# Kernel tuning notes

Measured on AMD Instinct MI355X. Metric: run time of the kernel, lower is better.

The kernel has to match this reference:

```python
import jax, jax.numpy as jnp
from jax import lax
import numpy as np

B, V, H, K, E = 256, 30000, 512, 200, 300
SH_ALPHA = 20.0
REC_W = 0.7
N_ITERS = 100       # fixed iteration budget (original caps at 5000; convergence check freezes updates)
STOP_THR = 0.005
BN_EPS = 1e-3


def setup_inputs() -> dict:
    key = jax.random.key(0)
    ks = jax.random.split(key, 8)
    n = lambda k, shape, scale: (jax.random.normal(k, shape, jnp.float32) * scale)
    return {
        "bows": jax.random.uniform(ks[0], (B, V), jnp.float32),
        "W1": n(ks[1], (H, V), 0.01),
        "b1": jnp.zeros((H,), jnp.float32),
        "W2": n(ks[2], (K, H), 0.05),
        "b2": jnp.zeros((K,), jnp.float32),
        "gamma": jnp.ones((K,), jnp.float32),
        "beta": jnp.zeros((K,), jnp.float32),
        "word_emb": n(ks[3], (V, E), 0.1),
        "topic_emb": n(ks[4], (K, E), 0.1),
    }


def _l2norm(x):
    return x / jnp.maximum(jnp.linalg.norm(x, axis=1, keepdims=True), 1e-12)


def _sinkhorn(cost, kernel, a, b):
    # a: [K,B], b: [V,B], kernel: [K,V]
    u0 = jnp.ones_like(a) / a.shape[0]
    v0 = jnp.ones_like(b)

    def body(carry, i):
        u, v, err = carry
        active = err > STOP_THR
        # u = a / (kernel @ (b / (u^T kernel)^T))
        u1 = a / (kernel @ (b / (u.T @ kernel).T))

        def check(_):
            v1 = b / (kernel.T @ u1)
            u2 = a / (kernel @ v1)
            bb = v1 * (kernel.T @ u2)
            e = jnp.max(jnp.sum(jnp.abs(bb - b), axis=0))
            return u2, v1, e

        # original does the v-refresh + err check when steps % 20 == 1 (steps = i+1)
        u1, v1, e1 = lax.cond(i % 20 == 0, check, lambda _: (u1, v, err), None)
        u = jnp.where(active, u1, u)
        v = jnp.where(active, v1, v)
        err = jnp.where(active, e1, err)
        return (u, v, err), None

    (u, v, _), _ = lax.scan(jax.checkpoint(body), (u0, v0, jnp.asarray(1.0, a.dtype)),
                            jnp.arange(N_ITERS))
    # per-document sinkhorn cost: sum_k u * ((kernel*cost) @ v)
    return jnp.sum(u * ((kernel * cost) @ v), axis=0)  # [B]


def reference(bows, W1, b1, W2, b2, gamma, beta, word_emb, topic_emb):
    # encoder (training-mode BN with batch stats; dropout disabled for determinism)
    h = jax.nn.relu(bows @ W1.T + b1)                      # [B,H]
    z = h @ W2.T + b2                                      # [B,K]
    mu = jnp.mean(z, axis=0)
    var = jnp.var(z, axis=0)                               # biased, as torch BN uses
    zn = gamma * (z - mu) / jnp.sqrt(var + BN_EPS) + beta
    doc_topic = jax.nn.softmax(zn, axis=1)                 # [B,K]

    topic_word = _l2norm(topic_emb) @ _l2norm(word_emb).T  # [K,V]
    cost = 1.0 - topic_word
    kernel = jnp.exp(-cost * SH_ALPHA)

    doc_word = jax.nn.softmax(bows, axis=1)                # [B,V]
    sinkhorn_loss = _sinkhorn(cost, kernel, doc_topic.T, doc_word.T).mean()

    rec_log_probs = jax.nn.log_softmax(doc_topic @ topic_word, axis=1)  # [B,V]
    reconstruction_loss = -(rec_log_probs * bows).sum(axis=1).mean()
    return REC_W * reconstruction_loss, sinkhorn_loss
```

## Files before the change

kernel.cpp:

```cpp
#include <hip/hip_runtime.h>
#include <math.h>

#define CDIV(a,b) (((a)+(b)-1)/(b))

typedef unsigned short u16;
typedef unsigned long long u64;
typedef __attribute__((ext_vector_type(8))) short bf16x8;
typedef __attribute__((ext_vector_type(4))) float f32x4;

constexpr int Bn = 256;
constexpr int Vn = 30000;
constexpr int Hn = 512;
constexpr int Kn = 200;
constexpr int En = 300;
constexpr int E3 = 320;
constexpr int Kp = 224;
constexpr int Vc = 224;
constexpr int NCH = 136;
constexpr int CPX = NCH / 8;
constexpr int Vpad = NCH * Vc;
constexpr int SW1 = 64;
constexpr int KSL = 480;
constexpr float ALPHA  = 20.0f;
constexpr float RECW   = 0.7f;
constexpr float THRC   = 0.005f;
constexpr float EPS_BN = 1e-3f;
constexpr int   NIT    = 100;

__device__ __forceinline__ float bf2f(u16 h) {
  union { unsigned u; float f; } c; c.u = (unsigned)h << 16; return c.f;
}
__device__ __forceinline__ u16 f2bf(float f) {
  union { float f; unsigned u; } c; c.f = f;
  return (u16)((c.u + 0x7fffu + ((c.u >> 16) & 1u)) >> 16);
}
__device__ __forceinline__ bf16x8 load8bf(const float* p) {
  float4 a = *(const float4*)p, b = *(const float4*)(p + 4);
  bf16x8 r;
  r[0] = (short)f2bf(a.x); r[1] = (short)f2bf(a.y);
  r[2] = (short)f2bf(a.z); r[3] = (short)f2bf(a.w);
  r[4] = (short)f2bf(b.x); r[5] = (short)f2bf(b.y);
  r[6] = (short)f2bf(b.z); r[7] = (short)f2bf(b.w);
  return r;
}

template<int MODE>
__global__ __launch_bounds__(256, 2)
void fusedAB(const u16* __restrict__ kernT, const u16* __restrict__ kernA,
             const u16* __restrict__ ub, const u16* __restrict__ bmb,
             u16* __restrict__ wout, const u16* __restrict__ win,
             u16* __restrict__ tpart, float* __restrict__ errp,
             const int* __restrict__ frozen)
{
  if (MODE != 3 && frozen[0]) return;
  const int bid = blockIdx.x;
  const int xcd = bid & 7, wid = bid >> 3;
  const int c = xcd * CPX + (wid >> 2), g = wid & 3;
  const int v0 = c * Vc, b0 = g * 64;
  const int tid = threadIdx.x;
  const int wv = tid >> 6, l = tid & 63, l15 = l & 15, lg = l >> 4;
  const int rloc = wv * 16 + l15;
  const int bcol = b0 + rloc;
  __shared__ u16 wlds[64 * Vc];
  char* wbase = (char*)wlds;
  const int sw = (rloc & 3) << 4;

  if (MODE != 3) {
    bf16x8 uf[7];
    {
      const u16* up = ub + (size_t)bcol * Kp + lg * 8;
#pragma unroll
      for (int ks = 0; ks < 7; ++ks) uf[ks] = *(const bf16x8*)(up + ks * 32);
    }
    float e = 0.f;
    for (int vt = 0; vt < Vc / 16; ++vt) {
      const u16* ktp = kernT + (size_t)(v0 + vt * 16 + l15) * Kp + lg * 8;
      f32x4 acc = {0.f, 0.f, 0.f, 0.f};
#pragma unroll
      for (int ks = 0; ks < 7; ++ks) {
        bf16x8 kf = *(const bf16x8*)(ktp + ks * 32);
        acc = __builtin_amdgcn_mfma_f32_16x16x32_bf16(kf, uf[ks], acc, 0, 0, 0);
      }
      const int vbase = v0 + vt * 16 + lg * 4;
      const size_t po = (size_t)bcol * Vpad + vbase;
      u64 bq = *(const u64*)(bmb + po);
      if (MODE == 2) {
        u64 wq = *(const u64*)(win + po);
#pragma unroll
        for (int r = 0; r < 4; ++r) {
          float bm = bf2f((u16)(bq >> (16 * r)));
          float wv_ = bf2f((u16)(wq >> (16 * r)));
          e += fabsf(wv_ * acc[r] - bm);
        }
      } else {
        u64 wq = 0;
#pragma unroll
        for (int r = 0; r < 4; ++r) {
          float bm = bf2f((u16)(bq >> (16 * r)));
          float w = (vbase + r < Vn) ? bm / acc[r] : 0.f;
          wq |= (u64)f2bf(w) << (16 * r);
        }
        *(u64*)(wbase + rloc * (Vc * 2) + ((vt * 32 + lg * 8) ^ sw)) = wq;
        if (MODE == 1) *(u64*)(wout + po) = wq;
      }
    }
    if (MODE == 2) {
      e += __shfl_xor(e, 16, 64);
      e += __shfl_xor(e, 32, 64);
      if (l < 16) errp[c * Bn + bcol] = e;
      return;
    }
    __syncthreads();
  }

  f32x4 accB[13];
#pragma unroll
  for (int mt = 0; mt < 13; ++mt) accB[mt] = (f32x4){0.f, 0.f, 0.f, 0.f};
  for (int vs = 0; vs < Vc / 32; ++vs) {
    bf16x8 wf;
    if (MODE == 3) wf = *(const bf16x8*)(win + (size_t)bcol * Vpad + v0 + vs * 32 + lg * 8);
    else wf = *(const bf16x8*)(wbase + rloc * (Vc * 2) + (((vs * 32 + lg * 8) * 2) ^ sw));
    const u16* kap = kernA + (size_t)l15 * Vpad + v0 + vs * 32 + lg * 8;
#pragma unroll
    for (int mt = 0; mt < 13; ++mt) {
      bf16x8 af = *(const bf16x8*)(kap + (size_t)mt * 16 * Vpad);
      accB[mt] = __builtin_amdgcn_mfma_f32_16x16x32_bf16(af, wf, accB[mt], 0, 0, 0);
    }
  }
#pragma unroll
  for (int mt = 0; mt < 13; ++mt) {
#pragma unroll
    for (int r = 0; r < 4; ++r) {
      int k = mt * 16 + lg * 4 + r;
      if (k < Kn) tpart[((size_t)c * Kn + k) * Bn + bcol] = f2bf(accB[mt][r]);
    }
  }
}

__global__ __launch_bounds__(256, 2)
void reconMF(const u16* __restrict__ costT, const u16* __restrict__ dtb,
             u16* __restrict__ rbuf)
{
  const int c = blockIdx.x, g = blockIdx.y;
  const int v0 = c * Vc, b0 = g * 64;
  const int tid = threadIdx.x;
  const int wv = tid >> 6, l = tid & 63, l15 = l & 15, lg = l >> 4;
  const int bcol = b0 + wv * 16 + l15;
  bf16x8 uf[7];
  {
    const u16* up = dtb + (size_t)bcol * Kp + lg * 8;
#pragma unroll
    for (int ks = 0; ks < 7; ++ks) uf[ks] = *(const bf16x8*)(up + ks * 32);
  }
  for (int vt = 0; vt < Vc / 16; ++vt) {
    const u16* ktp = costT + (size_t)(v0 + vt * 16 + l15) * Kp + lg * 8;
    f32x4 acc = {0.f, 0.f, 0.f, 0.f};
#pragma unroll
    for (int ks = 0; ks < 7; ++ks) {
      bf16x8 kf = *(const bf16x8*)(ktp + ks * 32);
      acc = __builtin_amdgcn_mfma_f32_16x16x32_bf16(kf, uf[ks], acc, 0, 0, 0);
    }
    const int vbase = v0 + vt * 16 + lg * 4;
    u64 q = 0;
#pragma unroll
    for (int r = 0; r < 4; ++r) q |= (u64)f2bf(1.f - acc[r]) << (16 * r);
    *(u64*)(rbuf + (size_t)bcol * Vpad + vbase) = q;
  }
}

__global__ __launch_bounds__(256)
void gemmTW(const u16* __restrict__ nth, const u16* __restrict__ ntl,
            const u16* __restrict__ nwh, const u16* __restrict__ nwl,
            u16* __restrict__ kern_bf, u16* __restrict__ kc_bf,
            u16* __restrict__ cost_bf)
{
  const int n0 = blockIdx.x * 64;
  const int tid = threadIdx.x;
  const int wv = tid >> 6, l = tid & 63, l15 = l & 15, lg = l >> 4;
  const int n = n0 + wv * 16 + l15;
  const bool nok = n < Vn;
  f32x4 acc[14];
#pragma unroll
  for (int mt = 0; mt < 14; ++mt) acc[mt] = (f32x4){0.f, 0.f, 0.f, 0.f};
  for (int kc = 0; kc < E3; kc += 32) {
    bf16x8 bh = {0,0,0,0,0,0,0,0}, bl = {0,0,0,0,0,0,0,0};
    if (nok) {
      const size_t o = (size_t)n * E3 + kc + lg * 8;
      bh = *(const bf16x8*)(nwh + o);
      bl = *(const bf16x8*)(nwl + o);
    }
#pragma unroll
    for (int mt = 0; mt < 14; ++mt) {
      const size_t ao = (size_t)(mt * 16 + l15) * E3 + kc + lg * 8;
      bf16x8 ah = *(const bf16x8*)(nth + ao);
      bf16x8 al = *(const bf16x8*)(ntl + ao);
      acc[mt] = __builtin_amdgcn_mfma_f32_16x16x32_bf16(ah, bh, acc[mt], 0, 0, 0);
      acc[mt] = __builtin_amdgcn_mfma_f32_16x16x32_bf16(ah, bl, acc[mt], 0, 0, 0);
      acc[mt] = __builtin_amdgcn_mfma_f32_16x16x32_bf16(al, bh, acc[mt], 0, 0, 0);
    }
  }
#pragma unroll
  for (int mt = 0; mt < 14; ++mt) {
#pragma unroll
    for (int r = 0; r < 4; ++r) {
      int k = mt * 16 + lg * 4 + r;
      float cf = 1.f - acc[mt][r];
      float kf = expf(-ALPHA * cf);
      size_t o = (size_t)k * Vpad + n;
      kern_bf[o] = f2bf(kf);
      kc_bf[o]   = f2bf(kf * cf);
      cost_bf[o] = f2bf(cf);
    }
  }
}

__global__ __launch_bounds__(256)
void gemmW1(const float* __restrict__ A, const float* __restrict__ B,
            float* __restrict__ part)
{
  const int bid = blockIdx.x;
  const int xcd = bid & 7, t = bid >> 3;
  const int s = xcd * 8 + (t >> 3);
  const int nx = t & 7;
  const int n0 = nx * 64, k0 = s * KSL;
  const int tid = threadIdx.x;
  const int wv = tid >> 6, l = tid & 63, l15 = l & 15, lg = l >> 4;
  f32x4 acc[4][4];
#pragma unroll
  for (int i = 0; i < 4; ++i)
#pragma unroll
    for (int j = 0; j < 4; ++j) acc[i][j] = (f32x4){0.f, 0.f, 0.f, 0.f};

  bf16x8 aA[4], bA[4], aB[4], bB[4];

#define LDW1(KC, AF, BF)                                                        \
  { const int kk_ = (KC) + lg * 8;                                              \
    const bool ok_ = kk_ < Vn;                                                  \
    _Pragma("unroll")                                                           \
    for (int mt = 0; mt < 4; ++mt) {                                            \
      const int m_ = wv * 64 + mt * 16 + l15;                                   \
      AF[mt] = ok_ ? load8bf(A + (size_t)m_ * Vn + kk_) : (bf16x8){0,0,0,0,0,0,0,0}; \
    }                                                                           \
    _Pragma("unroll")                                                           \
    for (int nt = 0; nt < 4; ++nt) {                                            \
      const int n_ = n0 + nt * 16 + l15;                                        \
      BF[nt] = ok_ ? load8bf(B + (size_t)n_ * Vn + kk_) : (bf16x8){0,0,0,0,0,0,0,0}; \
    } }

#define FMAW1(AF, BF)                                                           \
  _Pragma("unroll")                                                             \
  for (int mt = 0; mt < 4; ++mt)                                                \
    _Pragma("unroll")                                                           \
    for (int nt = 0; nt < 4; ++nt)                                              \
      acc[mt][nt] = __builtin_amdgcn_mfma_f32_16x16x32_bf16(AF[mt], BF[nt], acc[mt][nt], 0, 0, 0);

  LDW1(k0, aA, bA);
#pragma unroll
  for (int step = 0; step < KSL / 32; ++step) {
    if ((step & 1) == 0) {
      if (step + 1 < KSL / 32) LDW1(k0 + (step + 1) * 32, aB, bB);
      FMAW1(aA, bA);
    } else {
      if (step + 1 < KSL / 32) LDW1(k0 + (step + 1) * 32, aA, bA);
      FMAW1(aB, bB);
    }
  }
#undef LDW1
#undef FMAW1

#pragma unroll
  for (int mt = 0; mt < 4; ++mt)
#pragma unroll
    for (int nt = 0; nt < 4; ++nt)
#pragma unroll
      for (int r = 0; r < 4; ++r) {
        const int m = wv * 64 + mt * 16 + lg * 4 + r;
        const int n = n0 + nt * 16 + l15;
        part[(size_t)s * (Bn * Hn) + (size_t)m * Hn + n] = acc[mt][nt][r];
      }
}

__global__ void transposeK(const u16* __restrict__ src, u16* __restrict__ dst)
{
  __shared__ u16 t[32][33];
  int tx = threadIdx.x & 31, ty = threadIdx.x >> 5;
  int v0 = blockIdx.x * 32, k0 = blockIdx.y * 32;
#pragma unroll
  for (int r = 0; r < 4; ++r) t[ty + 8 * r][tx] = src[(size_t)(k0 + ty + 8 * r) * Vpad + v0 + tx];
  __syncthreads();
#pragma unroll
  for (int r = 0; r < 4; ++r) dst[(size_t)(v0 + ty + 8 * r) * Kp + k0 + tx] = t[tx][ty + 8 * r];
}

__global__ void convTemb(const float* __restrict__ temb, const float* __restrict__ rnT,
                         u16* __restrict__ nth, u16* __restrict__ ntl)
{
  int k = blockIdx.x, e = threadIdx.x;
  float v = (k < Kn && e < En) ? temb[(size_t)k * En + e] * rnT[k] : 0.f;
  u16 hi = f2bf(v);
  nth[(size_t)k * E3 + e] = hi;
  ntl[(size_t)k * E3 + e] = f2bf(v - bf2f(hi));
}

__global__ void convWemb(const float* __restrict__ wemb, const float* __restrict__ rnW,
                         u16* __restrict__ nwh, u16* __restrict__ nwl)
{
  for (size_t idx = (size_t)blockIdx.x * 256 + threadIdx.x; idx < (size_t)Vn * E3;
       idx += (size_t)gridDim.x * 256) {
    int v = (int)(idx / E3), e = (int)(idx - (size_t)v * E3);
    float x = (e < En) ? wemb[(size_t)v * En + e] * rnW[v] : 0.f;
    u16 hi = f2bf(x);
    nwh[idx] = hi;
    nwl[idx] = f2bf(x - bf2f(hi));
  }
}

__global__ __launch_bounds__(256)
void gemm_nt(const float* __restrict__ A, const float* __restrict__ Bm,
             float* __restrict__ P, int M, int N, int Kd)
{
  const int S = gridDim.z, s = blockIdx.z;
  const int k0 = (int)((long long)Kd * s / S);
  const int k1 = (int)((long long)Kd * (s + 1) / S);
  const int m0 = blockIdx.y * 64, n0 = blockIdx.x * 64;
  __shared__ float As[16][68];
  __shared__ float Bs[16][68];
  const int tid = threadIdx.x;
  const int tx = tid & 15, ty = tid >> 4;
  const int lrow = tid >> 2, lkg = (tid & 3) * 4;
  const int mi = m0 + lrow, ni = n0 + lrow;
  float acc[4][4] = {};
  for (int kc = k0; kc < k1; kc += 16) {
    float4 a4 = {0.f, 0.f, 0.f, 0.f}, b4 = {0.f, 0.f, 0.f, 0.f};
    if (mi < M) a4 = *(const float4*)&A[(size_t)mi * Kd + kc + lkg];
    if (ni < N) b4 = *(const float4*)&Bm[(size_t)ni * Kd + kc + lkg];
    As[lkg + 0][lrow] = a4.x; As[lkg + 1][lrow] = a4.y;
    As[lkg + 2][lrow] = a4.z; As[lkg + 3][lrow] = a4.w;
    Bs[lkg + 0][lrow] = b4.x; Bs[lkg + 1][lrow] = b4.y;
    Bs[lkg + 2][lrow] = b4.z; Bs[lkg + 3][lrow] = b4.w;
    __syncthreads();
#pragma unroll
    for (int kk = 0; kk < 16; ++kk) {
      float4 av = *(const float4*)&As[kk][ty * 4];
      float4 bv = *(const float4*)&Bs[kk][tx * 4];
      float a_[4] = {av.x, av.y, av.z, av.w};
      float b_[4] = {bv.x, bv.y, bv.z, bv.w};
#pragma unroll
      for (int i = 0; i < 4; ++i)
#pragma unroll
        for (int j = 0; j < 4; ++j)
          acc[i][j] += a_[i] * b_[j];
    }
    __syncthreads();
  }
  const size_t base = (size_t)s * M * N;
#pragma unroll
  for (int i = 0; i < 4; ++i) {
    int m = m0 + ty * 4 + i;
    if (m >= M) continue;
#pragma unroll
    for (int j = 0; j < 4; ++j) {
      int n = n0 + tx * 4 + j;
      if (n < N) P[base + (size_t)m * N + n] = acc[i][j];
    }
  }
}

__global__ void rowNorms(const float* __restrict__ X, float* __restrict__ rn, int R, int C)
{
  int wv = threadIdx.x >> 6, lane = threadIdx.x & 63;
  int r = blockIdx.x * 4 + wv;
  if (r >= R) return;
  float s = 0.f;
  for (int c = lane; c < C; c += 64) { float x = X[(size_t)r * C + c]; s += x * x; }
#pragma unroll
  for (int m = 32; m; m >>= 1) s += __shfl_xor(s, m, 64);
  if (lane == 0) rn[r] = 1.f / fmaxf(sqrtf(s), 1e-12f);
}

__global__ void epiH(const float* __restrict__ P, const float* __restrict__ b1,
                     float* __restrict__ h, int S)
{
  int i = blockIdx.x * blockDim.x + threadIdx.x;
  if (i >= Bn * Hn) return;
  float v = b1[i & (Hn - 1)];
#pragma unroll 8
  for (int s = 0; s < S; ++s) v += P[(size_t)s * Bn * Hn + i];
  h[i] = fmaxf(v, 0.f);
}

__global__ void bnStats(const float* __restrict__ P, const float* __restrict__ b2,
                        float* __restrict__ mu, float* __restrict__ ivar, int S)
{
  int k = blockIdx.x, b = threadIdx.x;
  float z = b2[k];
  for (int s = 0; s < S; ++s) z += P[((size_t)s * Bn + b) * Kn + k];
  __shared__ float r1[256], r2[256];
  r1[b] = z; r2[b] = z * z; __syncthreads();
  for (int st = 128; st; st >>= 1) {
    if (b < st) { r1[b] += r1[b + st]; r2[b] += r2[b + st]; }
    __syncthreads();
  }
  if (b == 0) {
    float m = r1[0] / Bn, v = r2[0] / Bn - (r1[0] / Bn) * (r1[0] / Bn);
    mu[k] = m; ivar[k] = rsqrtf(v + EPS_BN);
  }
}

__global__ void bnSoftmax(const float* __restrict__ P, const float* __restrict__ b2,
                          const float* __restrict__ mu, const float* __restrict__ ivar,
                          const float* __restrict__ gamma, const float* __restrict__ beta,
                          float* __restrict__ a, u16* __restrict__ dtb, int S)
{
  int b = blockIdx.x, k = threadIdx.x;
  float zn = -1e30f;
  if (k < Kn) {
    float z = b2[k];
    for (int s = 0; s < S; ++s) z += P[((size_t)s * Bn + b) * Kn + k];
    zn = gamma[k] * (z - mu[k]) * ivar[k] + beta[k];
  }
  __shared__ float red[256];
  red[k] = zn; __syncthreads();
  for (int st = 128; st; st >>= 1) { if (k < st) red[k] = fmaxf(red[k], red[k + st]); __syncthreads(); }
  float mx = red[0]; __syncthreads();
  float e = (k < Kn) ? expf(zn - mx) : 0.f;
  red[k] = e; __syncthreads();
  for (int st = 128; st; st >>= 1) { if (k < st) red[k] += red[k + st]; __syncthreads(); }
  float dt = e / red[0];
  if (k < Kn) a[(size_t)k * Bn + b] = dt;
  if (k < Kp) dtb[(size_t)b * Kp + k] = (k < Kn) ? f2bf(dt) : (u16)0;
}

__global__ __launch_bounds__(512)
void rowSoftmax2(const float* __restrict__ bows, u16* __restrict__ bmb)
{
  int b = blockIdx.x, t = threadIdx.x;
  const float4* row = (const float4*)(bows + (size_t)b * Vn);
  __shared__ float red[512];
  float mx = -1e30f;
  for (int v4 = t; v4 < Vn / 4; v4 += 512) {
    float4 x = row[v4];
    mx = fmaxf(mx, fmaxf(fmaxf(x.x, x.y), fmaxf(x.z, x.w)));
  }
  red[t] = mx; __syncthreads();
  for (int st = 256; st; st >>= 1) { if (t < st) red[t] = fmaxf(red[t], red[t + st]); __syncthreads(); }
  mx = red[0]; __syncthreads();
  float sum = 0.f;
  for (int v4 = t; v4 < Vn / 4; v4 += 512) {
    float4 x = row[v4];
    sum += expf(x.x - mx) + expf(x.y - mx) + expf(x.z - mx) + expf(x.w - mx);
  }
  red[t] = sum; __syncthreads();
  for (int st = 256; st; st >>= 1) { if (t < st) red[t] += red[t + st]; __syncthreads(); }
  float inv = 1.f / red[0];
  for (int v4 = t; v4 < Vn / 4; v4 += 512) {
    float4 x = row[v4];
    u64 q = (u64)f2bf(expf(x.x - mx) * inv)
          | ((u64)f2bf(expf(x.y - mx) * inv) << 16)
          | ((u64)f2bf(expf(x.z - mx) * inv) << 32)
          | ((u64)f2bf(expf(x.w - mx) * inv) << 48);
    *(u64*)(bmb + (size_t)b * Vpad + v4 * 4) = q;
  }
  for (int p = t; p < (Vpad - Vn) / 4; p += 512)
    *(u64*)(bmb + (size_t)b * Vpad + Vn + p * 4) = 0;
}

__global__ void initU2(u16* __restrict__ ub)
{
  int b = blockIdx.x, k = threadIdx.x;
  ub[(size_t)b * Kp + k] = (k < Kn) ? f2bf(1.f / Kn) : (u16)0;
}

__global__ __launch_bounds__(256)
void updateU2(const u16* __restrict__ tpart, const float* __restrict__ a,
              u16* __restrict__ ub, const int* __restrict__ frozen)
{
  if (frozen[0]) return;
  const int k = blockIdx.x;
  const int cg = threadIdx.x >> 6, q = threadIdx.x & 63;
  const int b0 = q * 4;
  f32x4 t = {0.f, 0.f, 0.f, 0.f};
  for (int c = cg * (NCH / 4); c < (cg + 1) * (NCH / 4); ++c) {
    u64 qd = *(const u64*)(tpart + ((size_t)c * Kn + k) * Bn + b0);
    t[0] += bf2f((u16)qd);         t[1] += bf2f((u16)(qd >> 16));
    t[2] += bf2f((u16)(qd >> 32)); t[3] += bf2f((u16)(qd >> 48));
  }
  __shared__ f32x4 red[4][64];
  red[cg][q] = t;
  __syncthreads();
  if (cg == 0) {
    f32x4 s = red[0][q];
#pragma unroll
    for (int gg = 1; gg < 4; ++gg) {
      f32x4 o = red[gg][q];
      s[0] += o[0]; s[1] += o[1]; s[2] += o[2]; s[3] += o[3];
    }
    float4 av = *(const float4*)&a[(size_t)k * Bn + b0];
    ub[(size_t)(b0 + 0) * Kp + k] = f2bf(av.x / s[0]);
    ub[(size_t)(b0 + 1) * Kp + k] = f2bf(av.y / s[1]);
    ub[(size_t)(b0 + 2) * Kp + k] = f2bf(av.z / s[2]);
    ub[(size_t)(b0 + 3) * Kp + k] = f2bf(av.w / s[3]);
  }
}

__global__ __launch_bounds__(256)
void sumT(const u16* __restrict__ tpart, float* __restrict__ t2)
{
  const int k = blockIdx.x;
  const int cg = threadIdx.x >> 6, q = threadIdx.x & 63;
  const int b0 = q * 4;
  f32x4 t = {0.f, 0.f, 0.f, 0.f};
  for (int c = cg * (NCH / 4); c < (cg + 1) * (NCH / 4); ++c) {
    u64 qd = *(const u64*)(tpart + ((size_t)c * Kn + k) * Bn + b0);
    t[0] += bf2f((u16)qd);         t[1] += bf2f((u16)(qd >> 16));
    t[2] += bf2f((u16)(qd >> 32)); t[3] += bf2f((u16)(qd >> 48));
  }
  __shared__ f32x4 red[4][64];
  red[cg][q] = t;
  __syncthreads();
  if (cg == 0) {
    f32x4 s = red[0][q];
#pragma unroll
    for (int gg = 1; gg < 4; ++gg) {
      f32x4 o = red[gg][q];
      s[0] += o[0]; s[1] += o[1]; s[2] += o[2]; s[3] += o[3];
    }
    float4 ov; ov.x = s[0]; ov.y = s[1]; ov.z = s[2]; ov.w = s[3];
    *(float4*)&t2[(size_t)k * Bn + b0] = ov;
  }
}

__global__ void errFin(const float* __restrict__ errp, int nc, int* __restrict__ frozen)
{
  if (frozen[0]) return;
  int b = threadIdx.x;
  float s = 0.f;
  for (int c = 0; c < nc; ++c) s += errp[(size_t)c * Bn + b];
  __shared__ float red[256];
  red[b] = s; __syncthreads();
  for (int st = 128; st; st >>= 1) { if (b < st) red[b] = fmaxf(red[b], red[b + st]); __syncthreads(); }
  if (b == 0 && red[0] <= THRC) frozen[0] = 1;
}

__global__ __launch_bounds__(512)
void recPass2(const u16* __restrict__ r, const float* __restrict__ bows,
              float* __restrict__ Lb)
{
  int b = blockIdx.x, t = threadIdx.x;
  const float m = 1.0f;
  const float4* br = (const float4*)(bows + (size_t)b * Vn);
  float se = 0.f, dot = 0.f, bs = 0.f;
  for (int v4 = t; v4 < Vn / 4; v4 += 512) {
    u64 q = *(const u64*)(r + (size_t)b * Vpad + v4 * 4);
    float4 w = br[v4];
    float x0 = bf2f((u16)q), x1 = bf2f((u16)(q >> 16));
    float x2 = bf2f((u16)(q >> 32)), x3 = bf2f((u16)(q >> 48));
    se  += expf(x0 - m) + expf(x1 - m) + expf(x2 - m) + expf(x3 - m);
    dot += w.x * x0 + w.y * x1 + w.z * x2 + w.w * x3;
    bs  += w.x + w.y + w.z + w.w;
  }
  __shared__ float red[512];
  red[t] = se; __syncthreads();
  for (int st = 256; st; st >>= 1) { if (t < st) red[t] += red[t + st]; __syncthreads(); }
  float seT = red[0]; __syncthreads();
  red[t] = dot; __syncthreads();
  for (int st = 256; st; st >>= 1) { if (t < st) red[t] += red[t + st]; __syncthreads(); }
  float dotT = red[0]; __syncthreads();
  red[t] = bs; __syncthreads();
  for (int st = 256; st; st >>= 1) { if (t < st) red[t] += red[t + st]; __syncthreads(); }
  if (t == 0) Lb[b] = dotT - (m + logf(seT)) * red[0];
}

__global__ void finalOut(const u16* __restrict__ ub, const float* __restrict__ t2,
                         const float* __restrict__ Lb, float* __restrict__ outp)
{
  int b = threadIdx.x;
  float sl = 0.f;
  for (int k = 0; k < Kn; ++k) sl += bf2f(ub[(size_t)b * Kp + k]) * t2[(size_t)k * Bn + b];
  __shared__ float r1[256], r2[256];
  r1[b] = sl; r2[b] = Lb[b]; __syncthreads();
  for (int st = 128; st; st >>= 1) {
    if (b < st) { r1[b] += r1[b + st]; r2[b] += r2[b + st]; }
    __syncthreads();
  }
  if (b == 0) {
    outp[0] = RECW * (-(r2[0] / (float)Bn));
    outp[1] = r1[0] / (float)Bn;
  }
}

extern "C" void kernel_launch(void* const* d_in, const int* in_sizes, int n_in,
                              void* d_out, int out_size, void* d_ws, size_t ws_size,
                              hipStream_t stream)
{
  const float* bows  = (const float*)d_in[0];
  const float* W1    = (const float*)d_in[1];
  const float* b1    = (const float*)d_in[2];
  const float* W2    = (const float*)d_in[3];
  const float* b2    = (const float*)d_in[4];
  const float* gamma = (const float*)d_in[5];
  const float* beta  = (const float*)d_in[6];
  const float* wemb  = (const float*)d_in[7];
  const float* temb  = (const float*)d_in[8];
  float* out = (float*)d_out;

  float* ws = (float*)d_ws;
  size_t off = 0;
  auto alloc = [&](size_t n) { float* p = ws + off; off += (n + 63) & ~(size_t)63; return p; };
  size_t r1_floats = (size_t)Vn * E3;
  if ((size_t)SW1 * Bn * Hn > r1_floats) r1_floats = (size_t)SW1 * Bn * Hn;
  float* R1      = alloc(r1_floats);
  u16*   kern_bf = (u16*)alloc(((size_t)Kp * Vpad + 1) / 2);
  u16*   kernT   = (u16*)alloc(((size_t)Vpad * Kp + 1) / 2);
  u16*   kc_bf   = (u16*)alloc(((size_t)Kp * Vpad + 1) / 2);
  u16*   cost_bf = (u16*)alloc(((size_t)Kp * Vpad + 1) / 2);
  u16*   costT   = (u16*)alloc(((size_t)Vpad * Kp + 1) / 2);
  u16*   nt_hi   = (u16*)alloc(((size_t)Kp * E3 + 1) / 2);
  u16*   nt_lo   = (u16*)alloc(((size_t)Kp * E3 + 1) / 2);
  u16*   ub_bf   = (u16*)alloc(((size_t)Bn * Kp + 1) / 2);
  u16*   dt_bf   = (u16*)alloc(((size_t)Bn * Kp + 1) / 2);
  u16*   tpart   = (u16*)alloc(((size_t)NCH * Kn * Bn + 1) / 2);
  float* w2buf   = alloc((size_t)4 * Bn * Kn);
  float* hbuf    = alloc((size_t)Bn * Hn);
  float* abuf    = alloc((size_t)Kn * Bn);
  float* t2      = alloc((size_t)Kn * Bn);
  float* rnT     = alloc(Kn);
  float* rnW     = alloc(Vn);
  float* mu      = alloc(Kn);
  float* ivar    = alloc(Kn);
  float* errp    = alloc((size_t)NCH * Bn);
  float* Lb      = alloc(Bn);
  int* frozen = (int*)(ws + off); off += 64;
  if (off * sizeof(float) > ws_size) return;
  u16*   nw_hi  = (u16*)R1;
  u16*   nw_lo  = nw_hi + (size_t)Vn * E3;
  float* w1part = R1;
  u16*   bm_bf  = (u16*)R1;
  u16*   vb_bf  = bm_bf + (size_t)Bn * Vpad;
  u16*   rbuf   = kern_bf;

  hipMemsetAsync(frozen, 0, sizeof(int), stream);

  rowNorms<<<CDIV(Kn, 4), 256, 0, stream>>>(temb, rnT, Kn, En);
  rowNorms<<<CDIV(Vn, 4), 256, 0, stream>>>(wemb, rnW, Vn, En);
  convTemb<<<Kp, E3, 0, stream>>>(temb, rnT, nt_hi, nt_lo);
  convWemb<<<4096, 256, 0, stream>>>(wemb, rnW, nw_hi, nw_lo);
  gemmTW<<<Vpad / 64, 256, 0, stream>>>(nt_hi, nt_lo, nw_hi, nw_lo, kern_bf, kc_bf, cost_bf);
  transposeK<<<dim3(Vpad / 32, Kp / 32), 256, 0, stream>>>(kern_bf, kernT);
  transposeK<<<dim3(Vpad / 32, Kp / 32), 256, 0, stream>>>(cost_bf, costT);

  gemmW1<<<8 * SW1, 256, 0, stream>>>(bows, W1, w1part);
  epiH<<<CDIV(Bn * Hn, 256), 256, 0, stream>>>(w1part, b1, hbuf, SW1);
  {
    dim3 g(CDIV(Kn, 64), CDIV(Bn, 64), 4);
    gemm_nt<<<g, 256, 0, stream>>>(hbuf, W2, w2buf, Bn, Kn, Hn);
  }
  bnStats<<<Kn, 256, 0, stream>>>(w2buf, b2, mu, ivar, 4);
  bnSoftmax<<<Bn, 256, 0, stream>>>(w2buf, b2, mu, ivar, gamma, beta, abuf, dt_bf, 4);
  rowSoftmax2<<<Bn, 512, 0, stream>>>(bows, bm_bf);
  initU2<<<Bn, Kp, 0, stream>>>(ub_bf);

  const int gF = NCH * 4;
  for (int it = 0; it < NIT; ++it) {
    fusedAB<0><<<gF, 256, 0, stream>>>(kernT, kern_bf, ub_bf, bm_bf, nullptr, nullptr, tpart, nullptr, frozen);
    updateU2<<<Kn, 256, 0, stream>>>(tpart, abuf, ub_bf, frozen);
    if (it % 20 == 0) {
      fusedAB<1><<<gF, 256, 0, stream>>>(kernT, kern_bf, ub_bf, bm_bf, vb_bf, nullptr, tpart, nullptr, frozen);
      updateU2<<<Kn, 256, 0, stream>>>(tpart, abuf, ub_bf, frozen);
      fusedAB<2><<<gF, 256, 0, stream>>>(kernT, kern_bf, ub_bf, bm_bf, nullptr, vb_bf, tpart, errp, frozen);
      errFin<<<1, 256, 0, stream>>>(errp, NCH, frozen);
    }
  }

  reconMF<<<dim3(NCH, Bn / 64), 256, 0, stream>>>(costT, dt_bf, rbuf);
  recPass2<<<Bn, 512, 0, stream>>>(rbuf, bows, Lb);

  fusedAB<3><<<gF, 256, 0, stream>>>(nullptr, kc_bf, ub_bf, nullptr, nullptr, vb_bf, tpart, nullptr, frozen);
  sumT<<<Kn, 256, 0, stream>>>(tpart, t2);
  finalOut<<<1, 256, 0, stream>>>(ub_bf, t2, Lb, out);
}
```

Before: 2.312 ms.

## Pack Sinkhorn partial sums as k-quads, add nontemporal streaming, resplit W1 GEMM

Changes the tpart partial-sum layout so each lane writes four consecutive k values as one 64-bit store instead of four scattered 16-bit stores. updateU2 and sumT now read and write in that packed layout, and updateU2 writes ub as one u64 per thread. Streaming loads and stores of doc-word, v, w and tpart use nontemporal hints to limit cache pollution. The W1 GEMM split-K is retuned to 120 slices of 256. The aim is less store and transaction overhead in the 100-iteration loop, at the cost of more partials for epiH to reduce.

```diff
diff --git a/kernel.cpp b/kernel.cpp
--- a/kernel.cpp
+++ b/kernel.cpp
@@ -19,8 +19,9 @@
 constexpr int NCH = 136;
 constexpr int CPX = NCH / 8;
 constexpr int Vpad = NCH * Vc;
-constexpr int SW1 = 64;
-constexpr int KSL = 480;
+constexpr int KQ = 50;
+constexpr int SW1 = 120;
+constexpr int KSL = 256;
 constexpr float ALPHA  = 20.0f;
 constexpr float RECW   = 0.7f;
 constexpr float THRC   = 0.005f;
@@ -83,9 +84,9 @@
       }
       const int vbase = v0 + vt * 16 + lg * 4;
       const size_t po = (size_t)bcol * Vpad + vbase;
-      u64 bq = *(const u64*)(bmb + po);
+      u64 bq = __builtin_nontemporal_load((const u64*)(bmb + po));
       if (MODE == 2) {
-        u64 wq = *(const u64*)(win + po);
+        u64 wq = __builtin_nontemporal_load((const u64*)(win + po));
 #pragma unroll
         for (int r = 0; r < 4; ++r) {
           float bm = bf2f((u16)(bq >> (16 * r)));
@@ -101,7 +102,7 @@
           wq |= (u64)f2bf(w) << (16 * r);
         }
         *(u64*)(wbase + rloc * (Vc * 2) + ((vt * 32 + lg * 8) ^ sw)) = wq;
-        if (MODE == 1) *(u64*)(wout + po) = wq;
+        if (MODE == 1) __builtin_nontemporal_store(wq, (u64*)(wout + po));
       }
     }
     if (MODE == 2) {
@@ -118,8 +119,15 @@
   for (int mt = 0; mt < 13; ++mt) accB[mt] = (f32x4){0.f, 0.f, 0.f, 0.f};
   for (int vs = 0; vs < Vc / 32; ++vs) {
     bf16x8 wf;
-    if (MODE == 3) wf = *(const bf16x8*)(win + (size_t)bcol * Vpad + v0 + vs * 32 + lg * 8);
-    else wf = *(const bf16x8*)(wbase + rloc * (Vc * 2) + (((vs * 32 + lg * 8) * 2) ^ sw));
+    if (MODE == 3) {
+      union { u64 q[2]; bf16x8 v; } wu;
+      const u64* wp = (const u64*)(win + (size_t)bcol * Vpad + v0 + vs * 32 + lg * 8);
+      wu.q[0] = __builtin_nontemporal_load(wp);
+      wu.q[1] = __builtin_nontemporal_load(wp + 1);
+      wf = wu.v;
+    } else {
+      wf = *(const bf16x8*)(wbase + rloc * (Vc * 2) + (((vs * 32 + lg * 8) * 2) ^ sw));
+    }
     const u16* kap = kernA + (size_t)l15 * Vpad + v0 + vs * 32 + lg * 8;
 #pragma unroll
     for (int mt = 0; mt < 13; ++mt) {
@@ -129,10 +137,13 @@
   }
 #pragma unroll
   for (int mt = 0; mt < 13; ++mt) {
-#pragma unroll
-    for (int r = 0; r < 4; ++r) {
-      int k = mt * 16 + lg * 4 + r;
-      if (k < Kn) tpart[((size_t)c * Kn + k) * Bn + bcol] = f2bf(accB[mt][r]);
+    const int kq = mt * 4 + lg;
+    if (kq < KQ) {
+      u64 q = (u64)f2bf(accB[mt][0])
+            | ((u64)f2bf(accB[mt][1]) << 16)
+            | ((u64)f2bf(accB[mt][2]) << 32)
+            | ((u64)f2bf(accB[mt][3]) << 48);
+      __builtin_nontemporal_store(q, (u64*)(tpart + (((size_t)c * KQ + kq) * Bn + bcol) * 4));
     }
   }
 }
@@ -220,7 +231,7 @@
 {
   const int bid = blockIdx.x;
   const int xcd = bid & 7, t = bid >> 3;
-  const int s = xcd * 8 + (t >> 3);
+  const int s = xcd * 15 + (t >> 3);
   const int nx = t & 7;
   const int n0 = nx * 64, k0 = s * KSL;
   const int tid = threadIdx.x;
@@ -476,57 +487,60 @@
               u16* __restrict__ ub, const int* __restrict__ frozen)
 {
   if (frozen[0]) return;
-  const int k = blockIdx.x;
-  const int cg = threadIdx.x >> 6, q = threadIdx.x & 63;
-  const int b0 = q * 4;
+  const int kq = blockIdx.x >> 2, bq = blockIdx.x & 3;
+  const int cg = threadIdx.x >> 6, bloc = threadIdx.x & 63;
+  const int b = bq * 64 + bloc;
   f32x4 t = {0.f, 0.f, 0.f, 0.f};
   for (int c = cg * (NCH / 4); c < (cg + 1) * (NCH / 4); ++c) {
-    u64 qd = *(const u64*)(tpart + ((size_t)c * Kn + k) * Bn + b0);
+    u64 qd = __builtin_nontemporal_load(
+        (const u64*)(tpart + (((size_t)c * KQ + kq) * Bn + b) * 4));
     t[0] += bf2f((u16)qd);         t[1] += bf2f((u16)(qd >> 16));
     t[2] += bf2f((u16)(qd >> 32)); t[3] += bf2f((u16)(qd >> 48));
   }
   __shared__ f32x4 red[4][64];
-  red[cg][q] = t;
+  red[cg][bloc] = t;
   __syncthreads();
   if (cg == 0) {
-    f32x4 s = red[0][q];
+    f32x4 s = red[0][bloc];
 #pragma unroll
     for (int gg = 1; gg < 4; ++gg) {
-      f32x4 o = red[gg][q];
+      f32x4 o = red[gg][bloc];
       s[0] += o[0]; s[1] += o[1]; s[2] += o[2]; s[3] += o[3];
     }
-    float4 av = *(const float4*)&a[(size_t)k * Bn + b0];
-    ub[(size_t)(b0 + 0) * Kp + k] = f2bf(av.x / s[0]);
-    ub[(size_t)(b0 + 1) * Kp + k] = f2bf(av.y / s[1]);
-    ub[(size_t)(b0 + 2) * Kp + k] = f2bf(av.z / s[2]);
-    ub[(size_t)(b0 + 3) * Kp + k] = f2bf(av.w / s[3]);
+    const int k0 = kq * 4;
+    u64 q = (u64)f2bf(a[(size_t)(k0 + 0) * Bn + b] / s[0])
+          | ((u64)f2bf(a[(size_t)(k0 + 1) * Bn + b] / s[1]) << 16)
+          | ((u64)f2bf(a[(size_t)(k0 + 2) * Bn + b] / s[2]) << 32)
+          | ((u64)f2bf(a[(size_t)(k0 + 3) * Bn + b] / s[3]) << 48);
+    *(u64*)(ub + (size_t)b * Kp + k0) = q;
   }
 }
 
 __global__ __launch_bounds__(256)
 void sumT(const u16* __restrict__ tpart, float* __restrict__ t2)
 {
-  const int k = blockIdx.x;
-  const int cg = threadIdx.x >> 6, q = threadIdx.x & 63;
-  const int b0 = q * 4;
+  const int kq = blockIdx.x >> 2, bq = blockIdx.x & 3;
+  const int cg = threadIdx.x >> 6, bloc = threadIdx.x & 63;
+  const int b = bq * 64 + bloc;
   f32x4 t = {0.f, 0.f, 0.f, 0.f};
   for (int c = cg * (NCH / 4); c < (cg + 1) * (NCH / 4); ++c) {
-    u64 qd = *(const u64*)(tpart + ((size_t)c * Kn + k) * Bn + b0);
+    u64 qd = __builtin_nontemporal_load(
+        (const u64*)(tpart + (((size_t)c * KQ + kq) * Bn + b) * 4));
     t[0] += bf2f((u16)qd);         t[1] += bf2f((u16)(qd >> 16));
     t[2] += bf2f((u16)(qd >> 32)); t[3] += bf2f((u16)(qd >> 48));
   }
   __shared__ f32x4 red[4][64];
-  red[cg][q] = t;
+  red[cg][bloc] = t;
   __syncthreads();
   if (cg == 0) {
-    f32x4 s = red[0][q];
+    f32x4 s = red[0][bloc];
 #pragma unroll
     for (int gg = 1; gg < 4; ++gg) {
-      f32x4 o = red[gg][q];
+      f32x4 o = red[gg][bloc];
       s[0] += o[0]; s[1] += o[1]; s[2] += o[2]; s[3] += o[3];
     }
     float4 ov; ov.x = s[0]; ov.y = s[1]; ov.z = s[2]; ov.w = s[3];
-    *(float4*)&t2[(size_t)k * Bn + b0] = ov;
+    *(float4*)&t2[(((size_t)kq * Bn) + b) * 4] = ov;
   }
 }
 
@@ -576,7 +590,8 @@
 {
   int b = threadIdx.x;
   float sl = 0.f;
-  for (int k = 0; k < Kn; ++k) sl += bf2f(ub[(size_t)b * Kp + k]) * t2[(size_t)k * Bn + b];
+  for (int k = 0; k < Kn; ++k)
+    sl += bf2f(ub[(size_t)b * Kp + k]) * t2[(((size_t)(k >> 2) * Bn) + b) * 4 + (k & 3)];
   __shared__ float r1[256], r2[256];
   r1[b] = sl; r2[b] = Lb[b]; __syncthreads();
   for (int st = 128; st; st >>= 1) {
@@ -619,11 +634,11 @@
   u16*   nt_lo   = (u16*)alloc(((size_t)Kp * E3 + 1) / 2);
   u16*   ub_bf   = (u16*)alloc(((size_t)Bn * Kp + 1) / 2);
   u16*   dt_bf   = (u16*)alloc(((size_t)Bn * Kp + 1) / 2);
-  u16*   tpart   = (u16*)alloc(((size_t)NCH * Kn * Bn + 1) / 2);
+  u16*   tpart   = (u16*)alloc(((size_t)NCH * KQ * Bn * 4 + 1) / 2);
   float* w2buf   = alloc((size_t)4 * Bn * Kn);
   float* hbuf    = alloc((size_t)Bn * Hn);
   float* abuf    = alloc((size_t)Kn * Bn);
-  float* t2      = alloc((size_t)Kn * Bn);
+  float* t2      = alloc((size_t)KQ * Bn * 4);
   float* rnT     = alloc(Kn);
   float* rnW     = alloc(Vn);
   float* mu      = alloc(Kn);
@@ -663,10 +678,10 @@
   const int gF = NCH * 4;
   for (int it = 0; it < NIT; ++it) {
     fusedAB<0><<<gF, 256, 0, stream>>>(kernT, kern_bf, ub_bf, bm_bf, nullptr, nullptr, tpart, nullptr, frozen);
-    updateU2<<<Kn, 256, 0, stream>>>(tpart, abuf, ub_bf, frozen);
+    updateU2<<<KQ * 4, 256, 0, stream>>>(tpart, abuf, ub_bf, frozen);
     if (it % 20 == 0) {
       fusedAB<1><<<gF, 256, 0, stream>>>(kernT, kern_bf, ub_bf, bm_bf, vb_bf, nullptr, tpart, nullptr, frozen);
-      updateU2<<<Kn, 256, 0, stream>>>(tpart, abuf, ub_bf, frozen);
+      updateU2<<<KQ * 4, 256, 0, stream>>>(tpart, abuf, ub_bf, frozen);
       fusedAB<2><<<gF, 256, 0, stream>>>(kernT, kern_bf, ub_bf, bm_bf, nullptr, vb_bf, tpart, errp, frozen);
       errFin<<<1, 256, 0, stream>>>(errp, NCH, frozen);
     }
@@ -676,6 +691,6 @@
   recPass2<<<Bn, 512, 0, stream>>>(rbuf, bows, Lb);
 
   fusedAB<3><<<gF, 256, 0, stream>>>(nullptr, kc_bf, ub_bf, nullptr, nullptr, vb_bf, tpart, nullptr, frozen);
-  sumT<<<Kn, 256, 0, stream>>>(tpart, t2);
+  sumT<<<KQ * 4, 256, 0, stream>>>(tpart, t2);
   finalOut<<<1, 256, 0, stream>>>(ub_bf, t2, Lb, out);
 }
```

After: 2.476 ms. 1.07x slower.
